# Performance work log

Hardware: AMD Instinct MI355X
Metric: run time of the kernel (lower is better)

Reference implementation:

```python
import jax, jax.numpy as jnp
import numpy as np

K = 32
TEMPERATURE = 1.0
EPS = 1e-12


def setup_inputs() -> dict:
    key = jax.random.key(0)
    k1, k2, k3, k4, k5 = jax.random.split(key, 5)
    N, F, B, H, C = 65536, 512, 2048, 256, 64
    X = jax.random.normal(k1, (N, F), dtype=jnp.float32)
    # non-negative PPR-like weights (dense representation of the sparse matrix)
    ppr_scores = jax.random.uniform(k2, (B, N), dtype=jnp.float32)
    s1 = 1.0 / np.sqrt(F)
    s2 = 1.0 / np.sqrt(H)
    W1 = jax.random.uniform(k3, (F, H), dtype=jnp.float32, minval=-s1, maxval=s1)
    W2 = jax.random.uniform(k4, (H, H), dtype=jnp.float32, minval=-s2, maxval=s2)
    W3 = jax.random.uniform(k5, (H, C), dtype=jnp.float32, minval=-s2, maxval=s2)
    return {"X": X, "ppr_scores": ppr_scores, "W1": W1, "W2": W2, "W3": W3}


def _mlp(X, W1, W2, W3):
    # PPRGoMLP, nlayers=3, no bias, dropout inactive at inference
    h = jnp.maximum(X @ W1, 0.0)
    h = jnp.maximum(h @ W2, 0.0)
    return h @ W3  # [N, C] logits


def _soft_k_medoid(A, x, k=K, temperature=TEMPERATURE, with_weight_correction=True):
    # A: [B, N] ppr weights, x: [N, C] embeddings
    topk_vals, topk_idx = jax.lax.top_k(A, k)          # [B, k]
    xk = x[topk_idx]                                    # [B, k, C] gathered neighbor embeddings
    # pairwise L2 distances among the top-k neighbors of each row: [B, k, k]
    d2 = jnp.sum(jnp.square(xk[:, :, None, :] - xk[:, None, :, :]), axis=-1)
    l2 = jnp.sqrt(d2 + EPS)
    # weighted sum of distances per candidate: [B, k]
    distances = jnp.einsum('bm,bcm->bc', topk_vals, l2)
    distances = jnp.where(topk_vals == 0, jnp.finfo(distances.dtype).max, distances)
    row_sum = jnp.sum(A, axis=-1, keepdims=True)        # [B, 1]
    w = jax.nn.softmax(-distances / temperature, axis=-1)
    if with_weight_correction:
        w = w * topk_vals
        w = w / jnp.sum(w, axis=-1, keepdims=True)
    return row_sum * jnp.einsum('bk,bkc->bc', w, xk)    # [B, C]


def reference(X, ppr_scores, W1, W2, W3):
    logits = _mlp(X, W1, W2, W3)
    return _soft_k_medoid(ppr_scores, logits)
```

## Files before the change

kernel.cpp:

```cpp
#include <hip/hip_runtime.h>
#include <hip/hip_bf16.h>

typedef unsigned short u16;
typedef __attribute__((ext_vector_type(8))) __bf16 bf16x8;
typedef __attribute__((ext_vector_type(4))) float f32x4;

#define AS1 __attribute__((address_space(1)))
#define AS3 __attribute__((address_space(3)))

__device__ inline void gload_lds16(const void* g, void* l) {
  __builtin_amdgcn_global_load_lds((const AS1 void*)g, (AS3 void*)l, 16, 0, 0);
}

__device__ inline u16 f2bf(float f) {
  __bf16 h = (__bf16)f;
  return __builtin_bit_cast(u16, h);
}

__device__ inline f32x4 ldnt(const f32x4* p) {
  return __builtin_nontemporal_load(p);
}

__global__ void conv_weights(const float* __restrict__ W1, const float* __restrict__ W2,
                             const float* __restrict__ W3, u16* __restrict__ w1t,
                             u16* __restrict__ w2t, u16* __restrict__ w3t) {
  int e = blockIdx.x * 256 + threadIdx.x;
  if (e < 131072) {
    int h = e >> 9, f = e & 511;
    w1t[e] = f2bf(W1[f * 256 + h]);
  } else if (e < 196608) {
    int x = e - 131072;
    int n = x >> 8, k = x & 255;
    w2t[x] = f2bf(W2[k * 256 + n]);
  } else if (e < 212992) {
    int x = e - 196608;
    int n = x >> 8, k = x & 255;
    w3t[x] = f2bf(W3[k * 64 + n]);
  }
}

__global__ __launch_bounds__(256, 2) void mlp_kernel(const float* __restrict__ X,
                                                     const u16* __restrict__ W1t,
                                                     const u16* __restrict__ W2t,
                                                     const u16* __restrict__ W3t,
                                                     float* __restrict__ lg) {
  __shared__ alignas(16) char smem[69632];
  u16* As   = (u16*)smem;
  u16* Bs   = (u16*)(smem + 4096);
  u16* h1s  = (u16*)(smem + 20480);
  u16* quad = (u16*)(smem + 53248);
  u16* w3s  = (u16*)(smem + 61440);
  const int bm = blockIdx.x, t = threadIdx.x;
  const int wid = t >> 6, lane = t & 63;
  const int wr = wid >> 1, wc = wid & 1;
  const int l15 = lane & 15, lk = lane >> 4;
  const f32x4 z = {0.f, 0.f, 0.f, 0.f};

  {
    f32x4 acc[2][8];
#pragma unroll
    for (int i = 0; i < 2; ++i)
#pragma unroll
      for (int j = 0; j < 8; ++j) acc[i][j] = z;

    for (int k0 = 0; k0 < 512; k0 += 32) {
#pragma unroll
      for (int it = 0; it < 4; ++it) {
        int s = it * 256 + t;
        gload_lds16(W1t + (size_t)(s >> 2) * 512 + k0 + (s & 3) * 8,
                    &Bs[(it * 256 + wid * 64) * 8]);
      }
      {
        const float* src = X + (size_t)(bm * 64 + (t >> 2)) * 512 + k0 + (t & 3) * 8;
        float4 v0 = *(const float4*)src;
        float4 v1 = *(const float4*)(src + 4);
        bf16x8 wv;
        wv[0] = (__bf16)v0.x; wv[1] = (__bf16)v0.y; wv[2] = (__bf16)v0.z; wv[3] = (__bf16)v0.w;
        wv[4] = (__bf16)v1.x; wv[5] = (__bf16)v1.y; wv[6] = (__bf16)v1.z; wv[7] = (__bf16)v1.w;
        *(bf16x8*)&As[t * 8] = wv;
      }
      __syncthreads();
      bf16x8 af[2], bfr[8];
#pragma unroll
      for (int i = 0; i < 2; ++i)
        af[i] = *(const bf16x8*)&As[(wr * 32 + i * 16 + l15) * 32 + lk * 8];
#pragma unroll
      for (int j = 0; j < 8; ++j)
        bfr[j] = *(const bf16x8*)&Bs[(wc * 128 + j * 16 + l15) * 32 + lk * 8];
#pragma unroll
      for (int i = 0; i < 2; ++i)
#pragma unroll
        for (int j = 0; j < 8; ++j)
          acc[i][j] = __builtin_amdgcn_mfma_f32_16x16x32_bf16(af[i], bfr[j], acc[i][j], 0, 0, 0);
      __syncthreads();
    }
#pragma unroll
    for (int i = 0; i < 2; ++i)
#pragma unroll
      for (int j = 0; j < 8; ++j)
#pragma unroll
        for (int r = 0; r < 4; ++r) {
          int row = wr * 32 + i * 16 + lk * 4 + r;
          int col = wc * 128 + j * 16 + l15;
          h1s[(row * 256 + col) ^ ((row & 7) << 3)] = f2bf(fmaxf(acc[i][j][r], 0.f));
        }
    __syncthreads();
  }

  f32x4 acc2[2][8];
#pragma unroll
  for (int i = 0; i < 2; ++i)
#pragma unroll
    for (int j = 0; j < 8; ++j) acc2[i][j] = z;

  for (int k0 = 0; k0 < 256; k0 += 32) {
#pragma unroll
    for (int it = 0; it < 4; ++it) {
      int s = it * 256 + t;
      gload_lds16(W2t + (size_t)(s >> 2) * 256 + k0 + (s & 3) * 8,
                  &Bs[(it * 256 + wid * 64) * 8]);
    }
    __syncthreads();
    bf16x8 af[2], bfr[8];
#pragma unroll
    for (int i = 0; i < 2; ++i) {
      int row = wr * 32 + i * 16 + l15;
      af[i] = *(const bf16x8*)&h1s[(row * 256 + k0 + lk * 8) ^ ((row & 7) << 3)];
    }
#pragma unroll
    for (int j = 0; j < 8; ++j)
      bfr[j] = *(const bf16x8*)&Bs[(wc * 128 + j * 16 + l15) * 32 + lk * 8];
#pragma unroll
    for (int i = 0; i < 2; ++i)
#pragma unroll
      for (int j = 0; j < 8; ++j)
        acc2[i][j] = __builtin_amdgcn_mfma_f32_16x16x32_bf16(af[i], bfr[j], acc2[i][j], 0, 0, 0);
    __syncthreads();
  }

  f32x4 acc3[4];
#pragma unroll
  for (int j = 0; j < 4; ++j) acc3[j] = z;

#pragma unroll
  for (int kk = 0; kk < 4; ++kk) {
    if (wc == (kk >> 1)) {
#pragma unroll
      for (int i = 0; i < 2; ++i)
#pragma unroll
        for (int j4 = 0; j4 < 4; ++j4) {
          int j = (kk & 1) * 4 + j4;
#pragma unroll
          for (int r = 0; r < 4; ++r) {
            int row = wr * 32 + i * 16 + lk * 4 + r;
            int c   = j4 * 16 + l15;
            quad[(row * 64 + c) ^ ((row & 7) << 3)] = f2bf(fmaxf(acc2[i][j][r], 0.f));
          }
        }
    }
#pragma unroll
    for (int it = 0; it < 2; ++it) {
      int s = it * 256 + t;
      int col = s >> 3;
      int koff = ((s ^ (col & 7)) & 7) * 8;
      gload_lds16(W3t + (size_t)col * 256 + kk * 64 + koff, &w3s[(it * 256 + wid * 64) * 8]);
    }
    __syncthreads();
    bf16x8 af2, bfr2[4];
#pragma unroll
    for (int ks = 0; ks < 2; ++ks) {
#pragma unroll
      for (int j2 = 0; j2 < 4; ++j2) {
        int col = j2 * 16 + l15;
        bfr2[j2] = *(const bf16x8*)&w3s[(col * 64 + ks * 32 + lk * 8) ^ ((col & 7) << 3)];
      }
      {
        int row = wid * 16 + l15;
        af2 = *(const bf16x8*)&quad[(row * 64 + ks * 32 + lk * 8) ^ ((row & 7) << 3)];
      }
#pragma unroll
      for (int j2 = 0; j2 < 4; ++j2)
        acc3[j2] = __builtin_amdgcn_mfma_f32_16x16x32_bf16(af2, bfr2[j2], acc3[j2], 0, 0, 0);
    }
    __syncthreads();
  }

#pragma unroll
  for (int j2 = 0; j2 < 4; ++j2) {
    int col = j2 * 16 + l15;
#pragma unroll
    for (int r = 0; r < 4; ++r) {
      int row = wid * 16 + lk * 4 + r;
      lg[(size_t)(bm * 64 + row) * 64 + col] = acc3[j2][r];
    }
  }
}

__global__ __launch_bounds__(256) void topk_medoid(const float* __restrict__ ppr,
                                                   const float* __restrict__ lg,
                                                   float* __restrict__ out) {
  __shared__ alignas(16) char smem[13312];
  float* cvals   = (float*)smem;
  int*   cidx    = (int*)(smem + 4096);
  float* xk      = (float*)smem;
  float* l2m     = (float*)(smem + 8448);
  float* vals    = (float*)(smem + 12672);
  int*   idxs    = (int*)(smem + 12800);
  float* dist    = (float*)(smem + 12928);
  float* wgt     = (float*)(smem + 13056);
  float* partial = (float*)(smem + 13184);
  int*   cnt     = (int*)(smem + 13200);
  float* rsum    = (float*)(smem + 13204);

  const int b = blockIdx.x, t = threadIdx.x;
  const int lane = t & 63, wid = t >> 6;
  const float* row = ppr + (size_t)b * 65536;
  const f32x4* rp = (const f32x4*)row;
  const float T0 = 0.997f;

  if (t == 0) *cnt = 0;
  __syncthreads();

  float sum = 0.f;
#pragma unroll 1
  for (int mb = 0; mb < 4; ++mb) {
    f32x4 v[16];
#pragma unroll
    for (int i = 0; i < 16; ++i) v[i] = ldnt(rp + (mb * 16 + i) * 256 + t);
#pragma unroll
    for (int i = 0; i < 16; ++i) {
      f32x4 x = v[i];
      sum += (x[0] + x[1]) + (x[2] + x[3]);
      float mx = fmaxf(fmaxf(x[0], x[1]), fmaxf(x[2], x[3]));
      if (mx > T0) {
        int fb = ((mb * 16 + i) * 256 + t) * 4;
#pragma unroll
        for (int j = 0; j < 4; ++j) {
          if (x[j] > T0) {
            int p = atomicAdd(cnt, 1);
            if (p < 1024) { cvals[p] = x[j]; cidx[p] = fb + j; }
          }
        }
      }
    }
  }
#pragma unroll
  for (int off = 32; off > 0; off >>= 1) sum += __shfl_down(sum, off);
  if (lane == 0) partial[wid] = sum;
  __syncthreads();

  const int ncand = *cnt;
  const int n = ncand < 1024 ? ncand : 1024;
  if (t == 0) *rsum = (partial[0] + partial[1]) + (partial[2] + partial[3]);

  if (n >= 32 && ncand <= 1024) {
    for (int p = t; p < n; p += 256) {
      float v = cvals[p];
      int id = cidx[p];
      int rank = 0;
      for (int q = 0; q < n; ++q) {
        float vq = cvals[q];
        int   iq = cidx[q];
        rank += (vq > v || (vq == v && iq < id)) ? 1 : 0;
      }
      if (rank < 32) { vals[rank] = v; idxs[rank] = id; }
    }
  } else if (wid == 0) {
    for (int r = 0; r < 32; ++r) {
      float bv = -__builtin_inff();
      int bi = 0x7fffffff;
      for (int p = lane; p < 65536; p += 64) {
        float xv = row[p];
        bool skip = false;
        for (int q = 0; q < r; ++q) skip = skip || (idxs[q] == p);
        if (!skip && (xv > bv || (xv == bv && p < bi))) { bv = xv; bi = p; }
      }
#pragma unroll
      for (int off = 32; off > 0; off >>= 1) {
        float ov = __shfl_down(bv, off);
        int   oi = __shfl_down(bi, off);
        if (ov > bv || (ov == bv && oi < bi)) { bv = ov; bi = oi; }
      }
      if (lane == 0) { vals[r] = bv; idxs[r] = bi; }
    }
  }
  __syncthreads();

  const float rs_b = *rsum;
#pragma unroll
  for (int j = 0; j < 8; ++j) {
    int s = j * 256 + t;
    int r = s >> 6, c = s & 63;
    xk[r * 65 + c] = lg[(size_t)idxs[r] * 64 + c];
  }
  __syncthreads();
#pragma unroll
  for (int j = 0; j < 4; ++j) {
    int p = j * 256 + t;
    int c = p >> 5, m = p & 31;
    float d = 0.f;
#pragma unroll
    for (int ch = 0; ch < 64; ++ch) {
      float df = xk[c * 65 + ch] - xk[m * 65 + ch];
      d += df * df;
    }
    l2m[c * 33 + m] = sqrtf(d + 1e-12f);
  }
  __syncthreads();
  if (t < 32) {
    float d = 0.f;
#pragma unroll
    for (int m = 0; m < 32; ++m) d += vals[m] * l2m[t * 33 + m];
    if (vals[t] == 0.f) d = 3.402823466e+38f;
    dist[t] = d;
  }
  __syncthreads();
  if (t == 0) {
    float mx = -3.402823466e+38f;
    for (int c = 0; c < 32; ++c) mx = fmaxf(mx, -dist[c]);
    float s = 0.f;
    for (int c = 0; c < 32; ++c) { float e = expf(-dist[c] - mx); wgt[c] = e; s += e; }
    float s2 = 0.f;
    for (int c = 0; c < 32; ++c) { wgt[c] = wgt[c] / s * vals[c]; s2 += wgt[c]; }
    float inv = 1.f / s2;
    for (int c = 0; c < 32; ++c) wgt[c] *= inv;
  }
  __syncthreads();
  if (t < 64) {
    float o = 0.f;
#pragma unroll
    for (int k = 0; k < 32; ++k) o += wgt[k] * xk[k * 65 + t];
    out[(size_t)b * 64 + t] = rs_b * o;
  }
}

extern "C" void kernel_launch(void* const* d_in, const int* in_sizes, int n_in,
                              void* d_out, int out_size, void* d_ws, size_t ws_size,
                              hipStream_t stream) {
  const float* X   = (const float*)d_in[0];
  const float* ppr = (const float*)d_in[1];
  const float* W1  = (const float*)d_in[2];
  const float* W2  = (const float*)d_in[3];
  const float* W3  = (const float*)d_in[4];
  float* out = (float*)d_out;
  char* ws = (char*)d_ws;

  u16*  w1t = (u16*)(ws + 0);
  u16*  w2t = (u16*)(ws + 262144);
  u16*  w3t = (u16*)(ws + 393216);
  float* lg = (float*)(ws + 458752);

  (void)in_sizes; (void)n_in; (void)out_size; (void)ws_size;

  conv_weights<<<832, 256, 0, stream>>>(W1, W2, W3, w1t, w2t, w3t);
  mlp_kernel<<<1024, 256, 0, stream>>>(X, w1t, w2t, w3t, lg);
  topk_medoid<<<2048, 256, 0, stream>>>(ppr, lg, out);
}
```

Measured before the change: 181.2 us.

## Double K-step to 64 with XOR-swizzled LDS tiles in MLP GEMMs

The MLP kernel's first two GEMMs now load a K-slice of 64 per iteration instead of 32, halving the number of loop iterations and barrier pairs. The A and B LDS tiles are XOR-swizzled by row to avoid bank conflicts on the wider rows. Shared memory is reorganised so quad and w3s alias the earlier A/B buffers, which grows LDS from 69632 to 73728 bytes per block. Larger LDS use per block could limit occupancy with launch_bounds(256,2).

```diff
diff --git a/kernel.cpp b/kernel.cpp
--- a/kernel.cpp
+++ b/kernel.cpp
@@ -44,12 +44,12 @@
                                                      const u16* __restrict__ W2t,
                                                      const u16* __restrict__ W3t,
                                                      float* __restrict__ lg) {
-  __shared__ alignas(16) char smem[69632];
+  __shared__ alignas(16) char smem[73728];
   u16* As   = (u16*)smem;
-  u16* Bs   = (u16*)(smem + 4096);
-  u16* h1s  = (u16*)(smem + 20480);
-  u16* quad = (u16*)(smem + 53248);
-  u16* w3s  = (u16*)(smem + 61440);
+  u16* Bs   = (u16*)(smem + 8192);
+  u16* h1s  = (u16*)(smem + 40960);
+  u16* quad = (u16*)smem;
+  u16* w3s  = (u16*)(smem + 8192);
   const int bm = blockIdx.x, t = threadIdx.x;
   const int wid = t >> 6, lane = t & 63;
   const int wr = wid >> 1, wc = wid & 1;
@@ -63,35 +63,46 @@
 #pragma unroll
       for (int j = 0; j < 8; ++j) acc[i][j] = z;
 
-    for (int k0 = 0; k0 < 512; k0 += 32) {
-#pragma unroll
-      for (int it = 0; it < 4; ++it) {
+    for (int k0 = 0; k0 < 512; k0 += 64) {
+#pragma unroll
+      for (int it = 0; it < 8; ++it) {
         int s = it * 256 + t;
-        gload_lds16(W1t + (size_t)(s >> 2) * 512 + k0 + (s & 3) * 8,
-                    &Bs[(it * 256 + wid * 64) * 8]);
-      }
-      {
-        const float* src = X + (size_t)(bm * 64 + (t >> 2)) * 512 + k0 + (t & 3) * 8;
+        int n = s >> 3;
+        int koff = ((s ^ (n & 7)) & 7) * 8;
+        gload_lds16(W1t + (size_t)n * 512 + k0 + koff, &Bs[s * 8]);
+      }
+#pragma unroll
+      for (int it = 0; it < 2; ++it) {
+        int s = it * 256 + t;
+        int row = s >> 3, c = s & 7;
+        const float* src = X + (size_t)(bm * 64 + row) * 512 + k0 + c * 8;
         float4 v0 = *(const float4*)src;
         float4 v1 = *(const float4*)(src + 4);
         bf16x8 wv;
         wv[0] = (__bf16)v0.x; wv[1] = (__bf16)v0.y; wv[2] = (__bf16)v0.z; wv[3] = (__bf16)v0.w;
         wv[4] = (__bf16)v1.x; wv[5] = (__bf16)v1.y; wv[6] = (__bf16)v1.z; wv[7] = (__bf16)v1.w;
-        *(bf16x8*)&As[t * 8] = wv;
+        *(bf16x8*)&As[(row * 64 + c * 8) ^ ((row & 7) << 3)] = wv;
       }
       __syncthreads();
-      bf16x8 af[2], bfr[8];
-#pragma unroll
-      for (int i = 0; i < 2; ++i)
-        af[i] = *(const bf16x8*)&As[(wr * 32 + i * 16 + l15) * 32 + lk * 8];
-#pragma unroll
-      for (int j = 0; j < 8; ++j)
-        bfr[j] = *(const bf16x8*)&Bs[(wc * 128 + j * 16 + l15) * 32 + lk * 8];
-#pragma unroll
-      for (int i = 0; i < 2; ++i)
-#pragma unroll
-        for (int j = 0; j < 8; ++j)
-          acc[i][j] = __builtin_amdgcn_mfma_f32_16x16x32_bf16(af[i], bfr[j], acc[i][j], 0, 0, 0);
+#pragma unroll
+      for (int ks = 0; ks < 2; ++ks) {
+        bf16x8 af[2], bfr[8];
+#pragma unroll
+        for (int i = 0; i < 2; ++i) {
+          int row = wr * 32 + i * 16 + l15;
+          af[i] = *(const bf16x8*)&As[(row * 64 + ks * 32 + lk * 8) ^ ((row & 7) << 3)];
+        }
+#pragma unroll
+        for (int j = 0; j < 8; ++j) {
+          int n = wc * 128 + j * 16 + l15;
+          bfr[j] = *(const bf16x8*)&Bs[(n * 64 + ks * 32 + lk * 8) ^ ((n & 7) << 3)];
+        }
+#pragma unroll
+        for (int i = 0; i < 2; ++i)
+#pragma unroll
+          for (int j = 0; j < 8; ++j)
+            acc[i][j] = __builtin_amdgcn_mfma_f32_16x16x32_bf16(af[i], bfr[j], acc[i][j], 0, 0, 0);
+      }
       __syncthreads();
     }
 #pragma unroll
@@ -113,28 +124,34 @@
 #pragma unroll
     for (int j = 0; j < 8; ++j) acc2[i][j] = z;
 
-  for (int k0 = 0; k0 < 256; k0 += 32) {
-#pragma unroll
-    for (int it = 0; it < 4; ++it) {
+  for (int k0 = 0; k0 < 256; k0 += 64) {
+#pragma unroll
+    for (int it = 0; it < 8; ++it) {
       int s = it * 256 + t;
-      gload_lds16(W2t + (size_t)(s >> 2) * 256 + k0 + (s & 3) * 8,
-                  &Bs[(it * 256 + wid * 64) * 8]);
-    }
-    __syncthreads();
-    bf16x8 af[2], bfr[8];
-#pragma unroll
-    for (int i = 0; i < 2; ++i) {
-      int row = wr * 32 + i * 16 + l15;
-      af[i] = *(const bf16x8*)&h1s[(row * 256 + k0 + lk * 8) ^ ((row & 7) << 3)];
-    }
-#pragma unroll
-    for (int j = 0; j < 8; ++j)
-      bfr[j] = *(const bf16x8*)&Bs[(wc * 128 + j * 16 + l15) * 32 + lk * 8];
-#pragma unroll
-    for (int i = 0; i < 2; ++i)
-#pragma unroll
-      for (int j = 0; j < 8; ++j)
-        acc2[i][j] = __builtin_amdgcn_mfma_f32_16x16x32_bf16(af[i], bfr[j], acc2[i][j], 0, 0, 0);
+      int n = s >> 3;
+      int koff = ((s ^ (n & 7)) & 7) * 8;
+      gload_lds16(W2t + (size_t)n * 256 + k0 + koff, &Bs[s * 8]);
+    }
+    __syncthreads();
+#pragma unroll
+    for (int ks = 0; ks < 2; ++ks) {
+      bf16x8 af[2], bfr[8];
+#pragma unroll
+      for (int i = 0; i < 2; ++i) {
+        int row = wr * 32 + i * 16 + l15;
+        af[i] = *(const bf16x8*)&h1s[(row * 256 + k0 + ks * 32 + lk * 8) ^ ((row & 7) << 3)];
+      }
+#pragma unroll
+      for (int j = 0; j < 8; ++j) {
+        int n = wc * 128 + j * 16 + l15;
+        bfr[j] = *(const bf16x8*)&Bs[(n * 64 + ks * 32 + lk * 8) ^ ((n & 7) << 3)];
+      }
+#pragma unroll
+      for (int i = 0; i < 2; ++i)
+#pragma unroll
+        for (int j = 0; j < 8; ++j)
+          acc2[i][j] = __builtin_amdgcn_mfma_f32_16x16x32_bf16(af[i], bfr[j], acc2[i][j], 0, 0, 0);
+    }
     __syncthreads();
   }
 
```

Measured after the change: 173.8 us. -4.1%, faster.
